# Performance work log

Measured on AMD Instinct MI355X. Metric: run time of the kernel, lower is better.

## Reference

```python
import jax, jax.numpy as jnp
import numpy as np

N = 50000        # nodes
E = 800000       # edges (avg degree 16)
F_IN = 128       # num_node_features
HEADS = 4        # const.NUM_HEADS
CH = 32          # const.NUM_CHANNELS
CLS = 40         # num_classes
NEG_SLOPE = 0.2  # PyG GATv2Conv default


def setup_inputs() -> dict:
    key = jax.random.key(0)
    ks = jax.random.split(key, 10)
    x = jax.random.normal(ks[0], (N, F_IN), dtype=jnp.float32)
    edge_index = jax.random.randint(ks[1], (2, E), 0, N, dtype=jnp.int64)
    s1 = 1.0 / np.sqrt(F_IN)
    s2 = 1.0 / np.sqrt(HEADS * CH)
    w1_l = jax.random.normal(ks[2], (F_IN, HEADS * CH), jnp.float32) * s1
    w1_r = jax.random.normal(ks[3], (F_IN, HEADS * CH), jnp.float32) * s1
    a1 = jax.random.normal(ks[4], (HEADS, CH), jnp.float32) * (1.0 / np.sqrt(CH))
    b1 = jnp.zeros((HEADS * CH,), jnp.float32)
    w2_l = jax.random.normal(ks[5], (HEADS * CH, CLS), jnp.float32) * s2
    w2_r = jax.random.normal(ks[6], (HEADS * CH, CLS), jnp.float32) * s2
    a2 = jax.random.normal(ks[7], (1, CLS), jnp.float32) * (1.0 / np.sqrt(CLS))
    b2 = jnp.zeros((CLS,), jnp.float32)
    return {"x": x, "edge_index": edge_index, "w1_l": w1_l, "w1_r": w1_r,
            "a1": a1, "b1": b1, "w2_l": w2_l, "w2_r": w2_r, "a2": a2, "b2": b2}


def _gatv2_conv(x, src, dst, wl, wr, a, b, concat):
    """GATv2Conv (PyG semantics, eval mode: no dropout).
    src -> lin_l, dst -> lin_r; e = a . LeakyReLU(x_l[src] + x_r[dst]);
    segment softmax over dst; out_i = sum_j alpha * x_l[src]."""
    H, C = a.shape
    n = x.shape[0]
    xl = (x @ wl).reshape(n, H, C)
    xr = (x @ wr).reshape(n, H, C)
    # per-edge additive attention logits [E, H]
    e = jnp.einsum('ehc,hc->eh', jax.nn.leaky_relu(xl[src] + xr[dst], NEG_SLOPE), a)
    # numerically stable segment softmax over target nodes
    m = jax.ops.segment_max(e, dst, num_segments=n)          # [n, H]
    p = jnp.exp(e - m[dst])
    denom = jax.ops.segment_sum(p, dst, num_segments=n)     # [n, H]
    alpha = p / denom[dst]
    out = jax.ops.segment_sum(alpha[..., None] * xl[src], dst, num_segments=n)  # [n, H, C]
    out = out.reshape(n, H * C) if concat else out.mean(axis=1)
    return out + b


def reference(x, edge_index, w1_l, w1_r, a1, b1, w2_l, w2_r, a2, b2):
    n = x.shape[0]
    # PyG GATv2Conv default add_self_loops=True
    loop = jnp.arange(n, dtype=edge_index.dtype)
    src = jnp.concatenate([edge_index[0], loop])
    dst = jnp.concatenate([edge_index[1], loop])
    h = jax.nn.elu(_gatv2_conv(x, src, dst, w1_l, w1_r, a1, b1, concat=True))
    # F.dropout with training=False is identity
    out = _gatv2_conv(h, src, dst, w2_l, w2_r, a2, b2, concat=False)
    return jax.nn.log_softmax(out, axis=1)
```

## Files before the change

kernel.cpp:

```cpp
#include <hip/hip_runtime.h>
#include <hip/hip_bf16.h>
#include <math.h>

#define NN 50000
#define NE 800000
#define ETOT (NE + NN)
#define CLS 40
#define CLSP 48
#define NEG 0.2f
#define MTILES (NN / 16)
#define GB1 ((MTILES + 3) / 4)
#define PREPB 176
#define NBUCK 196
#define BCAP 8192
#define EB 4096
#define KAB ((ETOT + EB - 1) / EB)
#define NHALF (NN / 2)
#define NODEB (NN / 8)

#define L2E 1.44269504088896f
#define C06 (0.6f * L2E)
#define C04 (0.4f * L2E)

typedef __hip_bfloat16 bf16;
typedef __attribute__((ext_vector_type(8))) __bf16 bf16x8;
typedef __attribute__((ext_vector_type(4))) float f32x4;
typedef __attribute__((ext_vector_type(2))) float f32x2;
struct U3 { unsigned x, y, z; };

__device__ __forceinline__ bf16x8 cvt8(f32x4 a, f32x4 b) {
    bf16x8 r;
    r[0] = (__bf16)a[0]; r[1] = (__bf16)a[1]; r[2] = (__bf16)a[2]; r[3] = (__bf16)a[3];
    r[4] = (__bf16)b[0]; r[5] = (__bf16)b[1]; r[6] = (__bf16)b[2]; r[7] = (__bf16)b[3];
    return r;
}
__device__ __forceinline__ f32x2 unpk2(unsigned u) {
    f32x2 r;
    r.x = __uint_as_float(u << 16);
    r.y = __uint_as_float(u & 0xffff0000u);
    return r;
}

__device__ __forceinline__ unsigned scan256(unsigned v, unsigned* wsum) {
    int t = threadIdx.x;
    int lane = t & 63, w = t >> 6;
    unsigned inc = v;
#pragma unroll
    for (int d = 1; d < 64; d <<= 1) {
        unsigned x = __shfl_up(inc, d);
        if (lane >= d) inc += x;
    }
    if (lane == 63) wsum[w] = inc;
    __syncthreads();
    unsigned woff = 0;
#pragma unroll
    for (int i = 0; i < 4; i++) woff += (i < w) ? wsum[i] : 0;
    return woff + inc - v;
}

__global__ __launch_bounds__(256) void prep(
        const float* __restrict__ w1l, const float* __restrict__ w1r,
        const float* __restrict__ w2l, const float* __restrict__ w2r,
        bf16* __restrict__ wT1, bf16* __restrict__ wT2,
        int* __restrict__ bcursor) {
    int t = blockIdx.x * 256 + threadIdx.x;
    if (t < NBUCK) bcursor[t] = 0;
    if (t < 2 * 128 * 128) {
        int m = t >> 14;
        int idx = t & 16383;
        int n = idx >> 7, k = idx & 127;
        const float* w = m ? w1r : w1l;
        wT1[t] = __float2bfloat16(w[k * 128 + n]);
    } else if (t < 2 * 128 * 128 + 2 * CLSP * 128) {
        int u = t - 2 * 128 * 128;
        int m = u / (CLSP * 128);
        int idx = u % (CLSP * 128);
        int n = idx >> 7, k = idx & 127;
        const float* w = m ? w2r : w2l;
        wT2[u] = __float2bfloat16((n < CLS) ? w[k * CLS + n] : 0.0f);
    }
}

__global__ __launch_bounds__(256) void gemm1_scatter(
        const float* __restrict__ x, const bf16* __restrict__ wT,
        bf16* __restrict__ outL, bf16* __restrict__ outR,
        const int* __restrict__ ei, int* __restrict__ bcursor,
        uint2* __restrict__ tmp) {
    __shared__ __align__(16) char smem[65536];
    if ((int)blockIdx.x < GB1) {
        const uint4* wsrc = (const uint4*)wT;
#pragma unroll
        for (int i = 0; i < 16; i++) {
            int idx = i * 256 + threadIdx.x;
            uint4 v = wsrc[idx];
            int r = idx >> 4;
            int c = (idx & 15) << 4;
            *(uint4*)(smem + r * 256 + (c ^ ((r & 7) << 4))) = v;
        }
        __syncthreads();
        int wave = threadIdx.x >> 6;
        int lane = threadIdx.x & 63;
        int tile = blockIdx.x * 4 + wave;
        if (tile >= MTILES) return;
        int row0 = tile * 16;
        int l16 = lane & 15, quad = lane >> 4;
        f32x4 z = {0.f, 0.f, 0.f, 0.f};
        f32x4 accl[8], accr[8];
#pragma unroll
        for (int i = 0; i < 8; i++) { accl[i] = z; accr[i] = z; }
        const float* xrow = x + (size_t)(row0 + l16) * 128 + quad * 8;
#pragma unroll
        for (int k0 = 0; k0 < 128; k0 += 32) {
            f32x4 a0 = *reinterpret_cast<const f32x4*>(xrow + k0);
            f32x4 a1v = *reinterpret_cast<const f32x4*>(xrow + k0 + 4);
            bf16x8 a = cvt8(a0, a1v);
            int cc = k0 * 2 + quad * 16;
#pragma unroll
            for (int ct = 0; ct < 8; ct++) {
                int rl = ct * 16 + l16;
                int sw = cc ^ ((l16 & 7) << 4);
                bf16x8 bl = *(const bf16x8*)(smem + rl * 256 + sw);
                bf16x8 br = *(const bf16x8*)(smem + 32768 + rl * 256 + sw);
                accl[ct] = __builtin_amdgcn_mfma_f32_16x16x32_bf16(a, bl, accl[ct], 0, 0, 0);
                accr[ct] = __builtin_amdgcn_mfma_f32_16x16x32_bf16(a, br, accr[ct], 0, 0, 0);
            }
        }
#pragma unroll
        for (int ct = 0; ct < 8; ct++)
#pragma unroll
            for (int r = 0; r < 4; r++) {
                size_t o = (size_t)(row0 + quad * 4 + r) * 128 + ct * 16 + l16;
                outL[o] = __float2bfloat16(accl[ct][r]);
                outR[o] = __float2bfloat16(accr[ct][r]);
            }
    } else {
        unsigned* hist   = (unsigned*)smem;
        unsigned* lstart = (unsigned*)(smem + 1024);
        unsigned* lcur   = (unsigned*)(smem + 2048);
        unsigned* gbase  = (unsigned*)(smem + 3072);
        unsigned* wsum   = (unsigned*)(smem + 4096);
        uint2*    binned = (uint2*)(smem + 4608);
        unsigned* target = (unsigned*)(smem + 37376);
        int t = threadIdx.x;
        int e0 = ((int)blockIdx.x - GB1) * EB;
        hist[t] = 0;
        __syncthreads();
        int srcs[16], dsts[16];
#pragma unroll
        for (int i = 0; i < 16; i++) {
            int e = e0 + i * 256 + t;
            if (e < ETOT) {
                int s, d;
                if (e < NE) { s = ei[e]; d = ei[NE + e]; }
                else        { s = d = e - NE; }
                srcs[i] = s; dsts[i] = d;
                atomicAdd(&hist[d >> 8], 1u);
            } else dsts[i] = -1;
        }
        __syncthreads();
        unsigned v = hist[t];
        unsigned excl = scan256(v, wsum);
        lstart[t] = excl;
        lcur[t] = 0;
        __syncthreads();
        if (t < NBUCK && v > 0)
            gbase[t] = (unsigned)atomicAdd(&bcursor[t], (int)v) + (unsigned)t * BCAP;
        __syncthreads();
#pragma unroll
        for (int i = 0; i < 16; i++) {
            int d = dsts[i];
            if (d >= 0) {
                int bk = d >> 8;
                unsigned p = atomicAdd(&lcur[bk], 1u);
                unsigned slot = lstart[bk] + p;
                binned[slot] = make_uint2((unsigned)srcs[i], (unsigned)d);
                target[slot] = gbase[bk] + p;
            }
        }
        __syncthreads();
        int tot = min(EB, ETOT - e0);
        for (int s = t; s < tot; s += 256)
            tmp[target[s]] = binned[s];
    }
}

__global__ __launch_bounds__(256) void bucket_sort(const int* __restrict__ bcursor,
                                                   const uint2* __restrict__ tmp,
                                                   int* __restrict__ csr_src,
                                                   int* __restrict__ startA,
                                                   int* __restrict__ degA,
                                                   int* __restrict__ row32) {
    __shared__ unsigned hist[256];
    __shared__ unsigned lstart[256];
    __shared__ unsigned lcur[256];
    __shared__ unsigned wsum[4];
    __shared__ int vals[BCAP];
    int b = blockIdx.x, t = threadIdx.x;
    int cnt = bcursor[b];
    hist[t] = 0;
    __syncthreads();
    const uint2* seg = tmp + (size_t)b * BCAP;
    for (int s = t; s < cnt; s += 256)
        atomicAdd(&hist[seg[s].y & 255], 1u);
    __syncthreads();
    unsigned v = hist[t];
    unsigned excl = scan256(v, wsum);
    lstart[t] = excl;
    lcur[t] = excl;
    int node = b * 256 + t;
    if (node < NN) {
        startA[node] = b * BCAP + (int)excl;
        degA[node] = (int)v;
    }
    __syncthreads();
    for (int s = t; s < cnt; s += 256) {
        uint2 p = seg[s];
        unsigned pos = atomicAdd(&lcur[p.y & 255], 1u);
        vals[pos] = (int)p.x;
    }
    __syncthreads();
    int* cbase = csr_src + (size_t)b * BCAP;
    for (int s = t; s < cnt; s += 256)
        cbase[s] = vals[s];
    int slot = t & 31;
#pragma unroll 4
    for (int i = 0; i < 32; i++) {
        int n2 = (t >> 5) + i * 8;
        int node2 = b * 256 + n2;
        if (node2 < NN) {
            int d2 = (int)hist[n2];
            int e2 = (int)lstart[n2];
            row32[(size_t)node2 * 32 + slot] = vals[e2 + min(slot, d2 - 1)];
        }
    }
}

struct L1S { float s; f32x2 acc[4]; };
__device__ __forceinline__ void l1_consume(uint4 u, bool valid, const f32x2* xrp,
                                           const f32x2* a06, const float* a04, L1S& st) {
    f32x2 t0 = unpk2(u.x) + xrp[0];
    f32x2 t1 = unpk2(u.y) + xrp[1];
    f32x2 t2 = unpk2(u.z) + xrp[2];
    f32x2 t3 = unpk2(u.w) + xrp[3];
    f32x2 ep = t0 * a06[0];
    ep = __builtin_elementwise_fma(t1, a06[1], ep);
    ep = __builtin_elementwise_fma(t2, a06[2], ep);
    ep = __builtin_elementwise_fma(t3, a06[3], ep);
    float e0 = fmaf(a04[1], fabsf(t0.y), a04[0] * fabsf(t0.x));
    e0 = fmaf(a04[2], fabsf(t1.x), e0);
    e0 = fmaf(a04[3], fabsf(t1.y), e0);
    float e1 = fmaf(a04[5], fabsf(t2.y), a04[4] * fabsf(t2.x));
    e1 = fmaf(a04[6], fabsf(t3.x), e1);
    e1 = fmaf(a04[7], fabsf(t3.y), e1);
    float e = (ep.x + ep.y) + (e0 + e1);
    e += __shfl_xor(e, 1);
    e += __shfl_xor(e, 2);
    float w = valid ? __builtin_amdgcn_exp2f(e) : 0.f;
    st.s += w;
    f32x2 wv = {w, w};
    st.acc[0] = __builtin_elementwise_fma(wv, t0, st.acc[0]);
    st.acc[1] = __builtin_elementwise_fma(wv, t1, st.acc[1]);
    st.acc[2] = __builtin_elementwise_fma(wv, t2, st.acc[2]);
    st.acc[3] = __builtin_elementwise_fma(wv, t3, st.acc[3]);
}

__global__ __launch_bounds__(256) void node_l1(const int* __restrict__ startA,
                                               const int* __restrict__ degA,
                                               const int* __restrict__ csr_src,
                                               const int* __restrict__ row32,
                                               const bf16* __restrict__ xl,
                                               const bf16* __restrict__ xr,
                                               const float* __restrict__ a1,
                                               const float* __restrict__ b1,
                                               bf16* __restrict__ hb,
                                               int nbase) {
    int wid = nbase + ((blockIdx.x * 256 + threadIdx.x) >> 6);
    int lane = threadIdx.x & 63;
    int g = lane >> 4, t = lane & 15;
    unsigned cB = (unsigned)t * 16;
    int deg = degA[wid];
    unsigned rowB = (unsigned)row32[((size_t)wid << 5) + (lane & 31)] << 8;
    const char* xlb = (const char*)xl;
    f32x2 xrp[4];
    {
        uint4 raw = *(const uint4*)((const char*)xr + ((unsigned)wid << 8) + cB);
        xrp[0] = unpk2(raw.x); xrp[1] = unpk2(raw.y);
        xrp[2] = unpk2(raw.z); xrp[3] = unpk2(raw.w);
    }
    f32x2 a06[4];
    float a04[8];
    {
        f32x4 lo = *reinterpret_cast<const f32x4*>(a1 + t * 8);
        f32x4 hi = *reinterpret_cast<const f32x4*>(a1 + t * 8 + 4);
        float af[8];
#pragma unroll
        for (int k = 0; k < 4; k++) { af[k] = lo[k]; af[k + 4] = hi[k]; }
#pragma unroll
        for (int j = 0; j < 4; j++) {
            a06[j].x = af[2 * j] * C06;
            a06[j].y = af[2 * j + 1] * C06;
        }
#pragma unroll
        for (int k = 0; k < 8; k++) a04[k] = af[k] * C04;
    }
    L1S st; st.s = 0.f;
    f32x2 z2 = {0.f, 0.f};
#pragma unroll
    for (int k = 0; k < 4; k++) st.acc[k] = z2;
    int nb = (deg + 3) >> 2;
    uint4 u[8];
#pragma unroll
    for (int i = 0; i < 4; i++) {
        int pp = min(i * 4 + g, deg - 1);
        u[i] = *(const uint4*)(xlb + (__shfl(rowB, pp) + cB));
    }
    if (nb > 4) {
#pragma unroll
        for (int i = 4; i < 8; i++) {
            int pp = min(i * 4 + g, deg - 1);
            u[i] = *(const uint4*)(xlb + (__shfl(rowB, pp) + cB));
        }
    }
    l1_consume(u[0], g < deg, xrp, a06, a04, st);
    if (nb > 1) l1_consume(u[1], 4 + g < deg, xrp, a06, a04, st);
    if (nb > 2) l1_consume(u[2], 8 + g < deg, xrp, a06, a04, st);
    if (nb > 3) l1_consume(u[3], 12 + g < deg, xrp, a06, a04, st);
    if (nb > 4) {
        l1_consume(u[4], 16 + g < deg, xrp, a06, a04, st);
        if (nb > 5) l1_consume(u[5], 20 + g < deg, xrp, a06, a04, st);
        if (nb > 6) l1_consume(u[6], 24 + g < deg, xrp, a06, a04, st);
        if (nb > 7) l1_consume(u[7], 28 + g < deg, xrp, a06, a04, st);
        if (nb > 8) {
            int j0t = startA[wid];
            for (int b = 8; b < nb; b++) {
                int p = b * 4 + g;
                bool valid = p < deg;
                int pp = valid ? p : deg - 1;
                unsigned o = (((unsigned)csr_src[j0t + pp]) << 8) + cB;
                uint4 uu = *(const uint4*)(xlb + o);
                l1_consume(uu, valid, xrp, a06, a04, st);
            }
        }
    }
#pragma unroll
    for (int d = 16; d < 64; d <<= 1) {
        st.s += __shfl_xor(st.s, d);
#pragma unroll
        for (int k = 0; k < 4; k++) {
            st.acc[k].x += __shfl_xor(st.acc[k].x, d);
            st.acc[k].y += __shfl_xor(st.acc[k].y, d);
        }
    }
    if (g == 0) {
        float inv = 1.f / st.s;
        unsigned pk[4];
#pragma unroll
        for (int k = 0; k < 4; k++) {
            float o0 = st.acc[k].x * inv - xrp[k].x + b1[t * 8 + 2 * k];
            float o1 = st.acc[k].y * inv - xrp[k].y + b1[t * 8 + 2 * k + 1];
            o0 = o0 > 0.f ? o0 : __expf(o0) - 1.f;
            o1 = o1 > 0.f ? o1 : __expf(o1) - 1.f;
            bf16 r0 = __float2bfloat16(o0), r1 = __float2bfloat16(o1);
            pk[k] = (unsigned)*reinterpret_cast<unsigned short*>(&r0) |
                    ((unsigned)*reinterpret_cast<unsigned short*>(&r1) << 16);
        }
        uint4 w4 = {pk[0], pk[1], pk[2], pk[3]};
        *(uint4*)((char*)hb + ((unsigned)wid << 8) + cB) = w4;
    }
}

__global__ __launch_bounds__(256) void gemm2(const bf16* __restrict__ h,
                                             const bf16* __restrict__ wT,
                                             bf16* __restrict__ outL,
                                             bf16* __restrict__ outR) {
    __shared__ __align__(16) char smem[24576];
    const uint4* wsrc = (const uint4*)wT;
#pragma unroll
    for (int i = 0; i < 6; i++) {
        int idx = i * 256 + threadIdx.x;
        uint4 v = wsrc[idx];
        int r = idx >> 4;
        int c = (idx & 15) << 4;
        *(uint4*)(smem + r * 256 + (c ^ ((r & 7) << 4))) = v;
    }
    __syncthreads();
    int wave = threadIdx.x >> 6;
    int lane = threadIdx.x & 63;
    int tile = blockIdx.x * 4 + wave;
    if (tile >= MTILES) return;
    int row0 = tile * 16;
    int l16 = lane & 15, quad = lane >> 4;
    f32x4 z = {0.f, 0.f, 0.f, 0.f};
    f32x4 accl[3], accr[3];
#pragma unroll
    for (int i = 0; i < 3; i++) { accl[i] = z; accr[i] = z; }
    const bf16* hrow = h + (size_t)(row0 + l16) * 128 + quad * 8;
#pragma unroll
    for (int k0 = 0; k0 < 128; k0 += 32) {
        bf16x8 a = *reinterpret_cast<const bf16x8*>(hrow + k0);
        int cc = k0 * 2 + quad * 16;
        int sw = cc ^ ((l16 & 7) << 4);
#pragma unroll
        for (int ct = 0; ct < 3; ct++) {
            int rl = ct * 16 + l16;
            bf16x8 bl = *(const bf16x8*)(smem + rl * 256 + sw);
            bf16x8 br = *(const bf16x8*)(smem + 12288 + rl * 256 + sw);
            accl[ct] = __builtin_amdgcn_mfma_f32_16x16x32_bf16(a, bl, accl[ct], 0, 0, 0);
            accr[ct] = __builtin_amdgcn_mfma_f32_16x16x32_bf16(a, br, accr[ct], 0, 0, 0);
        }
    }
#pragma unroll
    for (int ct = 0; ct < 3; ct++)
#pragma unroll
        for (int r = 0; r < 4; r++) {
            size_t o = (size_t)(row0 + quad * 4 + r) * CLSP + ct * 16 + l16;
            outL[o] = __float2bfloat16(accl[ct][r]);
            outR[o] = __float2bfloat16(accr[ct][r]);
        }
}

struct L2S { float s; f32x2 acc[3]; };
__device__ __forceinline__ void l2_consume(U3 u, bool valid, const f32x2* xrp,
                                           const f32x2* a06, const float* a04, L2S& st) {
    f32x2 t0 = unpk2(u.x) + xrp[0];
    f32x2 t1 = unpk2(u.y) + xrp[1];
    f32x2 t2 = unpk2(u.z) + xrp[2];
    f32x2 ep = t0 * a06[0];
    ep = __builtin_elementwise_fma(t1, a06[1], ep);
    ep = __builtin_elementwise_fma(t2, a06[2], ep);
    float es = fmaf(a04[1], fabsf(t0.y), a04[0] * fabsf(t0.x));
    es = fmaf(a04[2], fabsf(t1.x), es);
    es = fmaf(a04[3], fabsf(t1.y), es);
    es = fmaf(a04[4], fabsf(t2.x), es);
    es = fmaf(a04[5], fabsf(t2.y), es);
    float e = (ep.x + ep.y) + es;
    e += __shfl_xor(e, 1);
    e += __shfl_xor(e, 2);
    e += __shfl_xor(e, 4);
    float w = valid ? __builtin_amdgcn_exp2f(e) : 0.f;
    st.s += w;
    f32x2 wv = {w, w};
    st.acc[0] = __builtin_elementwise_fma(wv, t0, st.acc[0]);
    st.acc[1] = __builtin_elementwise_fma(wv, t1, st.acc[1]);
    st.acc[2] = __builtin_elementwise_fma(wv, t2, st.acc[2]);
}

__global__ __launch_bounds__(256) void node_l2(const int* __restrict__ startA,
                                               const int* __restrict__ degA,
                                               const int* __restrict__ csr_src,
                                               const int* __restrict__ row32,
                                               const bf16* __restrict__ xl2,
                                               const bf16* __restrict__ xr2,
                                               const float* __restrict__ a2,
                                               const float* __restrict__ b2,
                                               float* __restrict__ out) {
    int wv = (blockIdx.x * 256 + threadIdx.x) >> 6;
    int n0 = wv * 2, n1 = n0 + 1;
    int lane = threadIdx.x & 63;
    int g = lane >> 3, t = lane & 7;
    unsigned cB = (unsigned)t * 12;
    const char* xlb = (const char*)xl2;
    int c = t * 6;
    f32x2 a06[3];
    float a04[6], bv[6];
#pragma unroll
    for (int k = 0; k < 6; k++) {
        bool val = (c + k < CLS);
        float av = val ? a2[c + k] : 0.f;
        bv[k] = val ? b2[c + k] : 0.f;
        a04[k] = av * C04;
        if (k & 1) a06[k >> 1].y = av * C06; else a06[k >> 1].x = av * C06;
    }
    int dega = degA[n0], degb = degA[n1];
    unsigned rowBa = (unsigned)row32[((size_t)n0 << 5) + (lane & 31)] * 96u;
    unsigned rowBb = (unsigned)row32[((size_t)n1 << 5) + (lane & 31)] * 96u;
    f32x2 xra[3], xrb[3];
    {
        U3 ra = *(const U3*)((const char*)xr2 + (unsigned)n0 * 96u + cB);
        U3 rb = *(const U3*)((const char*)xr2 + (unsigned)n1 * 96u + cB);
        xra[0] = unpk2(ra.x); xra[1] = unpk2(ra.y); xra[2] = unpk2(ra.z);
        xrb[0] = unpk2(rb.x); xrb[1] = unpk2(rb.y); xrb[2] = unpk2(rb.z);
    }
    int nba = (dega + 7) >> 3, nbb = (degb + 7) >> 3;
    U3 ua[2], ub[2];
#pragma unroll
    for (int i = 0; i < 2; i++)
        ua[i] = *(const U3*)(xlb + (__shfl(rowBa, min(i * 8 + g, dega - 1)) + cB));
#pragma unroll
    for (int i = 0; i < 2; i++)
        ub[i] = *(const U3*)(xlb + (__shfl(rowBb, min(i * 8 + g, degb - 1)) + cB));
    L2S sa, sb;
    f32x2 z2 = {0.f, 0.f};
    sa.s = 0.f; sb.s = 0.f;
#pragma unroll
    for (int k = 0; k < 3; k++) { sa.acc[k] = z2; sb.acc[k] = z2; }
    l2_consume(ua[0], g < dega, xra, a06, a04, sa);
    if (nba > 1) l2_consume(ua[1], 8 + g < dega, xra, a06, a04, sa);
    U3 ua2[2];
    if (nba > 2) {
#pragma unroll
        for (int i = 0; i < 2; i++)
            ua2[i] = *(const U3*)(xlb + (__shfl(rowBa, min((i + 2) * 8 + g, dega - 1)) + cB));
    }
    l2_consume(ub[0], g < degb, xrb, a06, a04, sb);
    if (nbb > 1) l2_consume(ub[1], 8 + g < degb, xrb, a06, a04, sb);
    U3 ub2[2];
    if (nbb > 2) {
#pragma unroll
        for (int i = 0; i < 2; i++)
            ub2[i] = *(const U3*)(xlb + (__shfl(rowBb, min((i + 2) * 8 + g, degb - 1)) + cB));
    }
    if (nba > 2) {
        l2_consume(ua2[0], 16 + g < dega, xra, a06, a04, sa);
        if (nba > 3) l2_consume(ua2[1], 24 + g < dega, xra, a06, a04, sa);
        if (nba > 4) {
            int j0a = startA[n0];
            for (int b = 4; b < nba; b++) {
                int p = b * 8 + g;
                bool valid = p < dega;
                int pp = valid ? p : dega - 1;
                unsigned o = (unsigned)csr_src[j0a + pp] * 96u + cB;
                U3 uu = *(const U3*)(xlb + o);
                l2_consume(uu, valid, xra, a06, a04, sa);
            }
        }
    }
    if (nbb > 2) {
        l2_consume(ub2[0], 16 + g < degb, xrb, a06, a04, sb);
        if (nbb > 3) l2_consume(ub2[1], 24 + g < degb, xrb, a06, a04, sb);
        if (nbb > 4) {
            int j0b = startA[n1];
            for (int b = 4; b < nbb; b++) {
                int p = b * 8 + g;
                bool valid = p < degb;
                int pp = valid ? p : degb - 1;
                unsigned o = (unsigned)csr_src[j0b + pp] * 96u + cB;
                U3 uu = *(const U3*)(xlb + o);
                l2_consume(uu, valid, xrb, a06, a04, sb);
            }
        }
    }
#pragma unroll
    for (int d = 8; d < 64; d <<= 1) {
        sa.s += __shfl_xor(sa.s, d);
        sb.s += __shfl_xor(sb.s, d);
#pragma unroll
        for (int k = 0; k < 3; k++) {
            sa.acc[k].x += __shfl_xor(sa.acc[k].x, d);
            sa.acc[k].y += __shfl_xor(sa.acc[k].y, d);
            sb.acc[k].x += __shfl_xor(sb.acc[k].x, d);
            sb.acc[k].y += __shfl_xor(sb.acc[k].y, d);
        }
    }
    {
        float inv = 1.f / sa.s;
        float q[6];
        float mx = -3e38f;
#pragma unroll
        for (int k = 0; k < 6; k++) {
            bool val = (c + k < CLS);
            float av = (k & 1) ? sa.acc[k >> 1].y : sa.acc[k >> 1].x;
            float xv = (k & 1) ? xra[k >> 1].y : xra[k >> 1].x;
            q[k] = val ? (av * inv - xv + bv[k]) : -3e38f;
            mx = fmaxf(mx, q[k]);
        }
        mx = fmaxf(mx, __shfl_xor(mx, 1));
        mx = fmaxf(mx, __shfl_xor(mx, 2));
        mx = fmaxf(mx, __shfl_xor(mx, 4));
        float se = 0.f;
#pragma unroll
        for (int k = 0; k < 6; k++) if (c + k < CLS) se += __expf(q[k] - mx);
        se += __shfl_xor(se, 1);
        se += __shfl_xor(se, 2);
        se += __shfl_xor(se, 4);
        float ls = mx + __logf(se);
        if (g == 0) {
            float* o = out + (size_t)n0 * CLS + c;
#pragma unroll
            for (int k = 0; k < 6; k++)
                if (c + k < CLS) o[k] = q[k] - ls;
        }
    }
    {
        float inv = 1.f / sb.s;
        float q[6];
        float mx = -3e38f;
#pragma unroll
        for (int k = 0; k < 6; k++) {
            bool val = (c + k < CLS);
            float av = (k & 1) ? sb.acc[k >> 1].y : sb.acc[k >> 1].x;
            float xv = (k & 1) ? xrb[k >> 1].y : xrb[k >> 1].x;
            q[k] = val ? (av * inv - xv + bv[k]) : -3e38f;
            mx = fmaxf(mx, q[k]);
        }
        mx = fmaxf(mx, __shfl_xor(mx, 1));
        mx = fmaxf(mx, __shfl_xor(mx, 2));
        mx = fmaxf(mx, __shfl_xor(mx, 4));
        float se = 0.f;
#pragma unroll
        for (int k = 0; k < 6; k++) if (c + k < CLS) se += __expf(q[k] - mx);
        se += __shfl_xor(se, 1);
        se += __shfl_xor(se, 2);
        se += __shfl_xor(se, 4);
        float ls = mx + __logf(se);
        if (g == 0) {
            float* o = out + (size_t)n1 * CLS + c;
#pragma unroll
            for (int k = 0; k < 6; k++)
                if (c + k < CLS) o[k] = q[k] - ls;
        }
    }
}

extern "C" void kernel_launch(void* const* d_in, const int* in_sizes, int n_in,
                              void* d_out, int out_size, void* d_ws, size_t ws_size,
                              hipStream_t stream) {
    const float* x   = (const float*)d_in[0];
    const int*   ei  = (const int*)d_in[1];
    const float* w1l = (const float*)d_in[2];
    const float* w1r = (const float*)d_in[3];
    const float* a1  = (const float*)d_in[4];
    const float* b1  = (const float*)d_in[5];
    const float* w2l = (const float*)d_in[6];
    const float* w2r = (const float*)d_in[7];
    const float* a2  = (const float*)d_in[8];
    const float* b2  = (const float*)d_in[9];
    float* out = (float*)d_out;

    char* base = (char*)d_ws;
    int*   bcursor = (int*)(base + 0);
    int*   startA  = (int*)(base + 1024);
    int*   degA    = (int*)(base + 201024);
    uint2* tmp     = (uint2*)(base + 401024);
    int*   csr_src = (int*)(base + 13246080);
    bf16*  xl1     = (bf16*)(base + 19668608);
    bf16*  hb      = (bf16*)(base + 45268608);
    bf16*  xl2p    = (bf16*)(base + 58068608);
    bf16*  wT1     = (bf16*)(base + 67668608);
    bf16*  wT2     = (bf16*)(base + 67734144);
    int*   row32   = (int*)(base + 67758720);
    bf16* xr1  = xl1 + (size_t)NN * 128;
    bf16* xr2p = xl2p + (size_t)NN * CLSP;

    prep<<<PREPB, 256, 0, stream>>>(w1l, w1r, w2l, w2r, wT1, wT2, bcursor);
    gemm1_scatter<<<GB1 + KAB, 256, 0, stream>>>(x, wT1, xl1, xr1, ei, bcursor, tmp);
    bucket_sort<<<NBUCK, 256, 0, stream>>>(bcursor, tmp, csr_src, startA, degA, row32);
    node_l1<<<(NHALF * 64) / 256, 256, 0, stream>>>(startA, degA, csr_src, row32, xl1, xr1, a1, b1, hb, 0);
    node_l1<<<(NHALF * 64) / 256, 256, 0, stream>>>(startA, degA, csr_src, row32, xl1, xr1, a1, b1, hb, NHALF);
    gemm2<<<GB1, 256, 0, stream>>>(hb, wT2, xl2p, xr2p);
    node_l2<<<NODEB, 256, 0, stream>>>(startA, degA, csr_src, row32, xl2p, xr2p, a2, b2, out);
}
```

Baseline: 200.3 us.

## Pack binned edges into 32-bit words, write only CSR overflow, merge node_l1 launches

Result: faster. 195.8 us, median of 2 (-2.2%).

```diff
diff --git a/kernel.cpp b/kernel.cpp
--- a/kernel.cpp
+++ b/kernel.cpp
@@ -15,7 +15,6 @@
 #define BCAP 8192
 #define EB 4096
 #define KAB ((ETOT + EB - 1) / EB)
-#define NHALF (NN / 2)
 #define NODEB (NN / 8)
 
 #define L2E 1.44269504088896f
@@ -85,7 +84,7 @@
         const float* __restrict__ x, const bf16* __restrict__ wT,
         bf16* __restrict__ outL, bf16* __restrict__ outR,
         const int* __restrict__ ei, int* __restrict__ bcursor,
-        uint2* __restrict__ tmp) {
+        unsigned* __restrict__ tmp) {
     __shared__ __align__(16) char smem[65536];
     if ((int)blockIdx.x < GB1) {
         const uint4* wsrc = (const uint4*)wT;
@@ -139,8 +138,8 @@
         unsigned* lcur   = (unsigned*)(smem + 2048);
         unsigned* gbase  = (unsigned*)(smem + 3072);
         unsigned* wsum   = (unsigned*)(smem + 4096);
-        uint2*    binned = (uint2*)(smem + 4608);
-        unsigned* target = (unsigned*)(smem + 37376);
+        unsigned* binned = (unsigned*)(smem + 4608);
+        unsigned* target = (unsigned*)(smem + 20992);
         int t = threadIdx.x;
         int e0 = ((int)blockIdx.x - GB1) * EB;
         hist[t] = 0;
@@ -173,7 +172,7 @@
                 int bk = d >> 8;
                 unsigned p = atomicAdd(&lcur[bk], 1u);
                 unsigned slot = lstart[bk] + p;
-                binned[slot] = make_uint2((unsigned)srcs[i], (unsigned)d);
+                binned[slot] = ((unsigned)srcs[i] << 8) | ((unsigned)d & 255u);
                 target[slot] = gbase[bk] + p;
             }
         }
@@ -185,7 +184,7 @@
 }
 
 __global__ __launch_bounds__(256) void bucket_sort(const int* __restrict__ bcursor,
-                                                   const uint2* __restrict__ tmp,
+                                                   const unsigned* __restrict__ tmp,
                                                    int* __restrict__ csr_src,
                                                    int* __restrict__ startA,
                                                    int* __restrict__ degA,
@@ -199,9 +198,9 @@
     int cnt = bcursor[b];
     hist[t] = 0;
     __syncthreads();
-    const uint2* seg = tmp + (size_t)b * BCAP;
+    const unsigned* seg = tmp + (size_t)b * BCAP;
     for (int s = t; s < cnt; s += 256)
-        atomicAdd(&hist[seg[s].y & 255], 1u);
+        atomicAdd(&hist[seg[s] & 255u], 1u);
     __syncthreads();
     unsigned v = hist[t];
     unsigned excl = scan256(v, wsum);
@@ -214,14 +213,17 @@
     }
     __syncthreads();
     for (int s = t; s < cnt; s += 256) {
-        uint2 p = seg[s];
-        unsigned pos = atomicAdd(&lcur[p.y & 255], 1u);
-        vals[pos] = (int)p.x;
+        unsigned p = seg[s];
+        unsigned pos = atomicAdd(&lcur[p & 255u], 1u);
+        vals[pos] = (int)(p >> 8);
     }
     __syncthreads();
-    int* cbase = csr_src + (size_t)b * BCAP;
-    for (int s = t; s < cnt; s += 256)
-        cbase[s] = vals[s];
+    if (node < NN && v > 32) {
+        int* cb = csr_src + (size_t)b * BCAP;
+        int e2 = (int)excl;
+        for (int s2 = e2 + 32; s2 < e2 + (int)v; s2++)
+            cb[s2] = vals[s2];
+    }
     int slot = t & 31;
 #pragma unroll 4
     for (int i = 0; i < 32; i++) {
@@ -272,9 +274,8 @@
                                                const bf16* __restrict__ xr,
                                                const float* __restrict__ a1,
                                                const float* __restrict__ b1,
-                                               bf16* __restrict__ hb,
-                                               int nbase) {
-    int wid = nbase + ((blockIdx.x * 256 + threadIdx.x) >> 6);
+                                               bf16* __restrict__ hb) {
+    int wid = (blockIdx.x * 256 + threadIdx.x) >> 6;
     int lane = threadIdx.x & 63;
     int g = lane >> 4, t = lane & 15;
     unsigned cB = (unsigned)t * 16;
@@ -628,25 +629,24 @@
     float* out = (float*)d_out;
 
     char* base = (char*)d_ws;
-    int*   bcursor = (int*)(base + 0);
-    int*   startA  = (int*)(base + 1024);
-    int*   degA    = (int*)(base + 201024);
-    uint2* tmp     = (uint2*)(base + 401024);
-    int*   csr_src = (int*)(base + 13246080);
-    bf16*  xl1     = (bf16*)(base + 19668608);
-    bf16*  hb      = (bf16*)(base + 45268608);
-    bf16*  xl2p    = (bf16*)(base + 58068608);
-    bf16*  wT1     = (bf16*)(base + 67668608);
-    bf16*  wT2     = (bf16*)(base + 67734144);
-    int*   row32   = (int*)(base + 67758720);
+    int*      bcursor = (int*)(base + 0);
+    int*      startA  = (int*)(base + 1024);
+    int*      degA    = (int*)(base + 201024);
+    unsigned* tmp     = (unsigned*)(base + 401024);
+    int*      csr_src = (int*)(base + 6823552);
+    bf16*     xl1     = (bf16*)(base + 13246080);
+    bf16*     hb      = (bf16*)(base + 38846080);
+    bf16*     xl2p    = (bf16*)(base + 51646080);
+    bf16*     wT1     = (bf16*)(base + 61246080);
+    bf16*     wT2     = (bf16*)(base + 61311616);
+    int*      row32   = (int*)(base + 61336192);
     bf16* xr1  = xl1 + (size_t)NN * 128;
     bf16* xr2p = xl2p + (size_t)NN * CLSP;
 
     prep<<<PREPB, 256, 0, stream>>>(w1l, w1r, w2l, w2r, wT1, wT2, bcursor);
     gemm1_scatter<<<GB1 + KAB, 256, 0, stream>>>(x, wT1, xl1, xr1, ei, bcursor, tmp);
     bucket_sort<<<NBUCK, 256, 0, stream>>>(bcursor, tmp, csr_src, startA, degA, row32);
-    node_l1<<<(NHALF * 64) / 256, 256, 0, stream>>>(startA, degA, csr_src, row32, xl1, xr1, a1, b1, hb, 0);
-    node_l1<<<(NHALF * 64) / 256, 256, 0, stream>>>(startA, degA, csr_src, row32, xl1, xr1, a1, b1, hb, NHALF);
+    node_l1<<<(NN * 64) / 256, 256, 0, stream>>>(startA, degA, csr_src, row32, xl1, xr1, a1, b1, hb);
     gemm2<<<GB1, 256, 0, stream>>>(hb, wT2, xl2p, xr2p);
     node_l2<<<NODEB, 256, 0, stream>>>(startA, degA, csr_src, row32, xl2p, xr2p, a2, b2, out);
 }
```
